# Kernel optimization log

Hardware: AMD Instinct MI355X
Metric: run time of the kernel (lower is better)

The kernel has to match this reference:

```python
import jax, jax.numpy as jnp
import numpy as np

B, S, D = 2, 2048, 1024
H = 16
HD = D // H  # 64

def setup_inputs() -> dict:
    key = jax.random.key(0)
    ks = jax.random.split(key, 5)
    scale = 0.02
    x = jax.random.normal(ks[0], (B, S, D), dtype=jnp.float32)
    w_attn = jax.random.normal(ks[1], (D, 3 * D), dtype=jnp.float32) * scale
    b_attn = jnp.zeros((3 * D,), dtype=jnp.float32)
    w_proj = jax.random.normal(ks[2], (D, D), dtype=jnp.float32) * scale
    b_proj = jnp.zeros((D,), dtype=jnp.float32)
    return {"x": x, "w_attn": w_attn, "b_attn": b_attn, "w_proj": w_proj, "b_proj": b_proj}

def reference(x, w_attn, b_attn, w_proj, b_proj):
    b, s, d = x.shape
    qkv = x @ w_attn + b_attn                      # [B,S,3D]
    q, k, v = jnp.split(qkv, 3, axis=-1)
    # [B,H,S,HD]
    q = q.reshape(b, s, H, HD).transpose(0, 2, 1, 3)
    k = k.reshape(b, s, H, HD).transpose(0, 2, 1, 3)
    v = v.reshape(b, s, H, HD).transpose(0, 2, 1, 3)
    scores = jnp.einsum('bhqd,bhkd->bhqk', q, k) * (1.0 / np.sqrt(HD))
    causal = jnp.tril(jnp.ones((s, s), dtype=bool))
    scores = jnp.where(causal[None, None], scores, -jnp.inf)
    attn = jax.nn.softmax(scores, axis=-1)
    out = jnp.einsum('bhqk,bhkd->bhqd', attn, v)   # [B,H,S,HD]
    out = out.transpose(0, 2, 1, 3).reshape(b, s, d)
    return out @ w_proj + b_proj
```

## Files before the change

kernel.cpp:

```cpp
#include <hip/hip_runtime.h>

#define B_  2
#define S_  2048
#define D_  1024
#define H_  16
#define HD_ 64
#define TD_ 3072
#define M_  (B_*S_)
#define NWORK_ 24

using bf16x8 = __attribute__((ext_vector_type(8))) short;
using bf16x4 = __attribute__((ext_vector_type(4))) short;
using f32x4  = __attribute__((ext_vector_type(4))) float;

typedef __attribute__((address_space(1))) unsigned int uint_g;
typedef __attribute__((address_space(3))) unsigned int uint_l;

#define MFMA32 __builtin_amdgcn_mfma_f32_16x16x32_bf16

#if defined(__has_builtin)
#if __has_builtin(__builtin_amdgcn_mfma_f32_16x16x16_bf16_1k)
#define MFMA16(a,b,c) __builtin_amdgcn_mfma_f32_16x16x16_bf16_1k(a,b,c,0,0,0)
#define HAVE_MFMA16 1
#elif __has_builtin(__builtin_amdgcn_mfma_f32_16x16x16bf16_1k)
#define MFMA16(a,b,c) __builtin_amdgcn_mfma_f32_16x16x16bf16_1k(a,b,c,0,0,0)
#define HAVE_MFMA16 1
#endif
#endif
#ifndef HAVE_MFMA16
static __device__ __forceinline__ f32x4 MFMA16_stub(bf16x4 a, bf16x4 b, f32x4 c) { return c; }
#define MFMA16(a,b,c) MFMA16_stub(a,b,c)
#endif

static __device__ __forceinline__ short f2bf(float f) {
    unsigned u = __float_as_uint(f);
    u += 0x7FFFu + ((u >> 16) & 1u);
    return (short)(u >> 16);
}
static __device__ __forceinline__ unsigned pack2bf(float a, float b) {
    return (unsigned)(unsigned short)f2bf(a) | ((unsigned)(unsigned short)f2bf(b) << 16);
}
static __device__ __forceinline__ void gload_lds16(const short* g, short* l) {
    __builtin_amdgcn_global_load_lds((const uint_g*)g, (uint_l*)l, 16, 0, 0);
}
static __device__ __forceinline__ void unpack8(uint4 u, float* f) {
    unsigned a0 = u.x, a1 = u.y, a2 = u.z, a3 = u.w;
    f[0] = __uint_as_float(a0 << 16); f[1] = __uint_as_float(a0 & 0xFFFF0000u);
    f[2] = __uint_as_float(a1 << 16); f[3] = __uint_as_float(a1 & 0xFFFF0000u);
    f[4] = __uint_as_float(a2 << 16); f[5] = __uint_as_float(a2 & 0xFFFF0000u);
    f[6] = __uint_as_float(a3 << 16); f[7] = __uint_as_float(a3 & 0xFFFF0000u);
}

__global__ __launch_bounds__(256)
void prep_kernel(const float* __restrict__ x, short* __restrict__ xb,
                 const float* __restrict__ w_attn, short* __restrict__ wat,
                 const float* __restrict__ w_proj, short* __restrict__ wpt) {
    __shared__ float T[32][33];
    const int bx = blockIdx.x;
    if (bx < 4096) {
        int i = bx * 256 + threadIdx.x;
        float4 v = *((const float4*)x + i);
        short4 o;
        o.x = f2bf(v.x); o.y = f2bf(v.y); o.z = f2bf(v.z); o.w = f2bf(v.w);
        *((short4*)xb + i) = o;
        return;
    }
    const float* W; short* Wt; int N, n0, k0;
    if (bx < 7168) { int b = bx - 4096; W = w_attn; Wt = wat; N = TD_; n0 = (b % 96) * 32; k0 = (b / 96) * 32; }
    else           { int b = bx - 7168; W = w_proj; Wt = wpt; N = D_;  n0 = (b % 32) * 32; k0 = (b / 32) * 32; }
    const int tx = threadIdx.x & 31, ty = threadIdx.x >> 5;
    #pragma unroll
    for (int i = 0; i < 4; ++i)
        T[ty + i * 8][tx] = W[(size_t)(k0 + ty + i * 8) * N + n0 + tx];
    __syncthreads();
    #pragma unroll
    for (int i = 0; i < 4; ++i)
        Wt[(size_t)(n0 + ty + i * 8) * D_ + k0 + tx] = f2bf(T[tx][ty + i * 8]);
}

__global__ __launch_bounds__(256)
void vtrans_kernel(const short* __restrict__ V, short* __restrict__ Vt) {
    __shared__ short T[32][33];
    int p  = blockIdx.z;
    int s0 = blockIdx.x * 32;
    int d0 = blockIdx.y * 32;
    int tx = threadIdx.x & 31, ty = threadIdx.x >> 5;
    const short* Vp  = V  + (size_t)p * S_ * HD_;
    short*       Vtp = Vt + (size_t)p * HD_ * S_;
    #pragma unroll
    for (int i = 0; i < 4; ++i)
        T[ty + i * 8][tx] = Vp[(s0 + ty + i * 8) * HD_ + d0 + tx];
    __syncthreads();
    #pragma unroll
    for (int i = 0; i < 4; ++i)
        Vtp[(size_t)(d0 + ty + i * 8) * S_ + s0 + tx] = T[tx][ty + i * 8];
}

__global__ __launch_bounds__(256, 3)
void gemm128_qkv_kernel(const short* __restrict__ A, const short* __restrict__ Bt,
                        const float* __restrict__ bias,
                        short* __restrict__ Qo, short* __restrict__ Ko, short* __restrict__ Vo,
                        int M, int N, int K) {
    __shared__ __align__(16) char lds[49152];

    const int tid  = threadIdx.x;
    const int w    = tid >> 6, lane = tid & 63;
    const int quad = lane >> 4, l16 = lane & 15;
    const int wm   = w >> 1,  wn  = w & 1;

    const int gx  = gridDim.x;
    const int nwg = gx * gridDim.y;
    const int bid = blockIdx.y * gx + blockIdx.x;
    const int sbid = (bid & 7) * (nwg >> 3) + (bid >> 3);
    const int rowBase = (sbid / gx) * 128;
    const int colBase = (sbid % gx) * 128;

    const int scol = ((lane & 3) * 8) ^ ((lane & 32) >> 1);
    const int sr0  = w * 32 + (lane >> 2);
    const short* Asrc0 = A  + (size_t)(rowBase + sr0)      * K + scol;
    const short* Asrc1 = A  + (size_t)(rowBase + sr0 + 16) * K + scol;
    const short* Bsrc0 = Bt + (size_t)(colBase + sr0)      * K + scol;
    const short* Bsrc1 = Bt + (size_t)(colBase + sr0 + 16) * K + scol;

    const int rterm = (l16 * 64 + quad * 16) ^ ((l16 & 8) << 2);
    const char* ArdBase = lds + wm * 4096 + rterm;
    const char* BrdBase = lds + 24576 + wn * 4096 + rterm;

#define STAGE_A(t) { int sl_ = ((t) % 3) * 8192; \
    gload_lds16(Asrc0 + (size_t)(t) * 32, (short*)(lds + sl_) + (w * 2)     * 512); \
    gload_lds16(Asrc1 + (size_t)(t) * 32, (short*)(lds + sl_) + (w * 2 + 1) * 512); }
#define STAGE_B(t) { int sl_ = 24576 + ((t) % 3) * 8192; \
    gload_lds16(Bsrc0 + (size_t)(t) * 32, (short*)(lds + sl_) + (w * 2)     * 512); \
    gload_lds16(Bsrc1 + (size_t)(t) * 32, (short*)(lds + sl_) + (w * 2 + 1) * 512); }

    f32x4 acc[4][4];
    const f32x4 zero = {0.f, 0.f, 0.f, 0.f};
    #pragma unroll
    for (int i = 0; i < 4; ++i)
        #pragma unroll
        for (int j = 0; j < 4; ++j) acc[i][j] = zero;

    const int nk = K >> 5;
    STAGE_A(0); STAGE_B(0);
    STAGE_A(1); STAGE_B(1);

    for (int t = 0; t < nk; ++t) {
        if (t + 1 < nk) { asm volatile("s_waitcnt vmcnt(4)" ::: "memory"); }
        else            { asm volatile("s_waitcnt vmcnt(0)" ::: "memory"); }
        __builtin_amdgcn_s_barrier();
        __builtin_amdgcn_sched_barrier(0);

        const int sl = (t % 3) * 8192;
        const char* Ab = ArdBase + sl;
        const char* Bb = BrdBase + sl;
        bf16x8 bfr[4], afr[4];
        #pragma unroll
        for (int ni = 0; ni < 4; ++ni) bfr[ni] = *(const bf16x8*)(Bb + ni * 1024);
        #pragma unroll
        for (int mi = 0; mi < 4; ++mi) afr[mi] = *(const bf16x8*)(Ab + mi * 1024);
        if (t + 2 < nk) { STAGE_A(t + 2); STAGE_B(t + 2); }

        __builtin_amdgcn_s_setprio(1);
        #pragma unroll
        for (int mi = 0; mi < 4; ++mi)
            #pragma unroll
            for (int ni = 0; ni < 4; ++ni)
                acc[mi][ni] = MFMA32(afr[mi], bfr[ni], acc[mi][ni], 0, 0, 0);
        __builtin_amdgcn_s_setprio(0);
    }
#undef STAGE_A
#undef STAGE_B

    #pragma unroll
    for (int ni = 0; ni < 4; ++ni) {
        int col = colBase + wn * 64 + ni * 16 + l16;
        int sel = col >> 10, cr = col & 1023;
        int h = cr >> 6, d = cr & 63;
        float bv  = bias[col];
        short* dst = (sel == 0) ? Qo : (sel == 1) ? Ko : Vo;
        float  scl = (sel == 0) ? 0.125f * 1.44269504f : 1.0f;
        #pragma unroll
        for (int mi = 0; mi < 4; ++mi) {
            int row = rowBase + wm * 64 + mi * 16 + quad * 4;
            #pragma unroll
            for (int r = 0; r < 4; ++r) {
                int rw = row + r;
                int bb = rw >> 11, s = rw & 2047;
                dst[((size_t)(bb * H_ + h) * S_ + s) * HD_ + d] =
                    f2bf((acc[mi][ni][r] + bv) * scl);
            }
        }
    }
}

__global__ __launch_bounds__(256, 2)
void gemm128_ring_kernel(const short* __restrict__ A, const short* __restrict__ Bt,
                         const float* __restrict__ bias, float* __restrict__ Cf,
                         int M, int N, int K) {
    __shared__ __align__(16) char lds[65536];

    const int tid  = threadIdx.x;
    const int w    = tid >> 6, lane = tid & 63;
    const int quad = lane >> 4, l16 = lane & 15;
    const int wm   = w >> 1,  wn  = w & 1;

    const int gx  = gridDim.x;
    const int nwg = gx * gridDim.y;
    const int bid = blockIdx.y * gx + blockIdx.x;
    const int sbid = (bid & 7) * (nwg >> 3) + (bid >> 3);
    const int rowBase = (sbid / gx) * 128;
    const int colBase = (sbid % gx) * 128;

    const int scol = ((lane & 3) * 8) ^ ((lane & 32) >> 1);
    const int sr0  = w * 32 + (lane >> 2);
    const short* Asrc0 = A  + (size_t)(rowBase + sr0)      * K + scol;
    const short* Asrc1 = A  + (size_t)(rowBase + sr0 + 16) * K + scol;
    const short* Bsrc0 = Bt + (size_t)(colBase + sr0)      * K + scol;
    const short* Bsrc1 = Bt + (size_t)(colBase + sr0 + 16) * K + scol;

    const int rterm = (l16 * 64 + quad * 16) ^ ((l16 & 8) << 2);
    const char* ArdBase = lds + wm * 4096 + rterm;
    const char* BrdBase = lds + 32768 + wn * 4096 + rterm;

#define STAGE_A(t) { int sl_ = ((t) & 3) * 8192; \
    gload_lds16(Asrc0 + (size_t)(t) * 32, (short*)(lds + sl_) + (w * 2)     * 512); \
    gload_lds16(Asrc1 + (size_t)(t) * 32, (short*)(lds + sl_) + (w * 2 + 1) * 512); }
#define STAGE_B(t) { int sl_ = 32768 + ((t) & 3) * 8192; \
    gload_lds16(Bsrc0 + (size_t)(t) * 32, (short*)(lds + sl_) + (w * 2)     * 512); \
    gload_lds16(Bsrc1 + (size_t)(t) * 32, (short*)(lds + sl_) + (w * 2 + 1) * 512); }

    f32x4 acc[4][4];
    const f32x4 zero = {0.f, 0.f, 0.f, 0.f};
    #pragma unroll
    for (int i = 0; i < 4; ++i)
        #pragma unroll
        for (int j = 0; j < 4; ++j) acc[i][j] = zero;

    const int nk = K >> 5;
    STAGE_A(0); STAGE_B(0);
    STAGE_A(1); STAGE_B(1);

    for (int t = 0; t < nk; ++t) {
        if (t + 1 < nk) { asm volatile("s_waitcnt vmcnt(4)" ::: "memory"); }
        else            { asm volatile("s_waitcnt vmcnt(0)" ::: "memory"); }
        __builtin_amdgcn_s_barrier();
        __builtin_amdgcn_sched_barrier(0);

        const char* Ab = ArdBase + (t & 3) * 8192;
        const char* Bb = BrdBase + (t & 3) * 8192;
        bf16x8 bfr[4], afr[4];
        #pragma unroll
        for (int ni = 0; ni < 4; ++ni) bfr[ni] = *(const bf16x8*)(Bb + ni * 1024);
        #pragma unroll
        for (int mi = 0; mi < 4; ++mi) afr[mi] = *(const bf16x8*)(Ab + mi * 1024);
        if (t + 2 < nk) { STAGE_A(t + 2); STAGE_B(t + 2); }

        __builtin_amdgcn_s_setprio(1);
        #pragma unroll
        for (int mi = 0; mi < 4; ++mi)
            #pragma unroll
            for (int ni = 0; ni < 4; ++ni)
                acc[mi][ni] = MFMA32(afr[mi], bfr[ni], acc[mi][ni], 0, 0, 0);
        __builtin_amdgcn_s_setprio(0);
    }
#undef STAGE_A
#undef STAGE_B

    #pragma unroll
    for (int mi = 0; mi < 4; ++mi) {
        int row = rowBase + wm * 64 + mi * 16 + quad * 4;
        #pragma unroll
        for (int ni = 0; ni < 4; ++ni) {
            int col = colBase + wn * 64 + ni * 16 + l16;
            float bv = bias[col];
            #pragma unroll
            for (int r = 0; r < 4; ++r)
                Cf[(size_t)(row + r) * N + col] = acc[mi][ni][r] + bv;
        }
    }
}

__global__ __launch_bounds__(256, 3)
void flash_mfma_kernel(const short* __restrict__ Qg, const short* __restrict__ Kg,
                       const short* __restrict__ Vtg,
                       short* __restrict__ pO, float* __restrict__ pl) {
    __shared__ __align__(16) short Ks[64][72];
    __shared__ __align__(16) short Vs[64][72];

    const int plane_id = blockIdx.x;
    const int y = blockIdx.y;
    int qi, kc;
    if (y < 8) { qi = y; kc = 0; }
    else       { qi = 8 + ((y - 8) >> 1); kc = (y - 8) & 1; }
    int nkt = 2 * qi + 2 - kc * 16;
    if (nkt > 16) nkt = 16;
    const int kvOrigin = kc * 1024;

    const int tid  = threadIdx.x;
    const int w    = tid >> 6, lane = tid & 63;
    const int quad = lane >> 4, l16 = lane & 15;
    const int qBase = qi * 128;
    const size_t plane = (size_t)plane_id * S_ * HD_;

    const int sr0 = tid >> 3;
    const int sc0 = (tid & 7) * 8;

    const int qsubA = qBase + w * 32;
    const short* QrowA = Qg + plane + (size_t)(qsubA + l16) * HD_ + quad * 8;
    const bf16x8 qa0 = *(const bf16x8*)(QrowA);
    const bf16x8 qa1 = *(const bf16x8*)(QrowA + 32);
    const short* QrowB = QrowA + 16 * HD_;
    const bf16x8 qb0 = *(const bf16x8*)(QrowB);
    const bf16x8 qb1 = *(const bf16x8*)(QrowB + 32);

    f32x4 oA[4], oB[4];
    const f32x4 zero = {0.f, 0.f, 0.f, 0.f};
    #pragma unroll
    for (int i = 0; i < 4; ++i) { oA[i] = zero; oB[i] = zero; }
    float lA = 0.f, lB = 0.f;
    const int q_globA = qsubA + l16;
    const int q_globB = qsubA + 16 + l16;
    const int q_wave_max = qsubA + 31;

    uint4 ka0, ka1, va0, va1;
    ka0 = *(const uint4*)(Kg  + plane + (size_t)(kvOrigin + sr0)      * HD_ + sc0);
    ka1 = *(const uint4*)(Kg  + plane + (size_t)(kvOrigin + sr0 + 32) * HD_ + sc0);
    va0 = *(const uint4*)(Vtg + plane + (size_t)sr0        * S_ + kvOrigin + sc0);
    va1 = *(const uint4*)(Vtg + plane + (size_t)(sr0 + 32) * S_ + kvOrigin + sc0);

    for (int j = 0; j < nkt; ++j) {
        __syncthreads();
        *(uint4*)&Ks[sr0][sc0]      = ka0;
        *(uint4*)&Ks[sr0 + 32][sc0] = ka1;
        *(uint4*)&Vs[sr0][sc0]      = va0;
        *(uint4*)&Vs[sr0 + 32][sc0] = va1;
        __syncthreads();

        if (j + 1 < nkt) {
            const int kvB = kvOrigin + (j + 1) * 64;
            ka0 = *(const uint4*)(Kg  + plane + (size_t)(kvB + sr0)      * HD_ + sc0);
            ka1 = *(const uint4*)(Kg  + plane + (size_t)(kvB + sr0 + 32) * HD_ + sc0);
            va0 = *(const uint4*)(Vtg + plane + (size_t)sr0        * S_ + kvB + sc0);
            va1 = *(const uint4*)(Vtg + plane + (size_t)(sr0 + 32) * S_ + kvB + sc0);
        }

        const int kvBase = kvOrigin + j * 64;
        if (kvBase > q_wave_max) continue;

        f32x4 sA[4], sB[4];
        __builtin_amdgcn_s_setprio(1);
        #pragma unroll
        for (int ct = 0; ct < 4; ++ct) {
            bf16x8 kf0 = *(const bf16x8*)&Ks[ct * 16 + l16][quad * 8];
            bf16x8 kf1 = *(const bf16x8*)&Ks[ct * 16 + l16][32 + quad * 8];
            f32x4 a = zero, b = zero;
            a = MFMA32(kf0, qa0, a, 0, 0, 0);
            a = MFMA32(kf1, qa1, a, 0, 0, 0);
            b = MFMA32(kf0, qb0, b, 0, 0, 0);
            b = MFMA32(kf1, qb1, b, 0, 0, 0);
            sA[ct] = a; sB[ct] = b;
        }
        __builtin_amdgcn_s_setprio(0);

        if (kvBase + 63 > qsubA) {
            #pragma unroll
            for (int ct = 0; ct < 4; ++ct) {
                int kv = kvBase + ct * 16 + quad * 4;
                #pragma unroll
                for (int r = 0; r < 4; ++r)
                    if (kv + r > q_globA) sA[ct][r] = -3.0e38f;
            }
        }
        if (kvBase + 63 > qsubA + 16) {
            #pragma unroll
            for (int ct = 0; ct < 4; ++ct) {
                int kv = kvBase + ct * 16 + quad * 4;
                #pragma unroll
                for (int r = 0; r < 4; ++r)
                    if (kv + r > q_globB) sB[ct][r] = -3.0e38f;
            }
        }

        #pragma unroll
        for (int ct = 0; ct < 4; ++ct) {
            float pa0 = __builtin_amdgcn_exp2f(sA[ct][0]), pa1 = __builtin_amdgcn_exp2f(sA[ct][1]);
            float pa2 = __builtin_amdgcn_exp2f(sA[ct][2]), pa3 = __builtin_amdgcn_exp2f(sA[ct][3]);
            float pb0 = __builtin_amdgcn_exp2f(sB[ct][0]), pb1 = __builtin_amdgcn_exp2f(sB[ct][1]);
            float pb2 = __builtin_amdgcn_exp2f(sB[ct][2]), pb3 = __builtin_amdgcn_exp2f(sB[ct][3]);
            lA += (pa0 + pa1) + (pa2 + pa3);
            lB += (pb0 + pb1) + (pb2 + pb3);
            bf16x4 pA, pB;
            *(unsigned*)&pA       = pack2bf(pa0, pa1);
            *((unsigned*)&pA + 1) = pack2bf(pa2, pa3);
            *(unsigned*)&pB       = pack2bf(pb0, pb1);
            *((unsigned*)&pB + 1) = pack2bf(pb2, pb3);
            __builtin_amdgcn_s_setprio(1);
            #pragma unroll
            for (int dt = 0; dt < 4; ++dt) {
                bf16x4 vfr = *(const bf16x4*)&Vs[dt * 16 + l16][ct * 16 + quad * 4];
                oA[dt] = MFMA16(vfr, pA, oA[dt]);
                oB[dt] = MFMA16(vfr, pB, oB[dt]);
            }
            __builtin_amdgcn_s_setprio(0);
        }
    }

    lA += __shfl_xor(lA, 16); lA += __shfl_xor(lA, 32);
    lB += __shfl_xor(lB, 16); lB += __shfl_xor(lB, 32);
    const size_t lbase = ((size_t)plane_id * NWORK_ + y) * 128 + w * 32;
    if (quad == 0) {
        pl[lbase + l16]      = lA;
        pl[lbase + 16 + l16] = lB;
    }

    __syncthreads();
    short* Pw = (w < 2) ? &Ks[w * 32][0] : &Vs[(w - 2) * 32][0];
    #pragma unroll
    for (int dt = 0; dt < 4; ++dt) {
        uint2 ua, ub;
        ua.x = pack2bf(oA[dt][0], oA[dt][1]);
        ua.y = pack2bf(oA[dt][2], oA[dt][3]);
        ub.x = pack2bf(oB[dt][0], oB[dt][1]);
        ub.y = pack2bf(oB[dt][2], oB[dt][3]);
        *(uint2*)&Pw[l16 * 72 + dt * 16 + quad * 4]        = ua;
        *(uint2*)&Pw[(16 + l16) * 72 + dt * 16 + quad * 4] = ub;
    }
    __builtin_amdgcn_s_waitcnt(0xC07F);
    short* outBase = pO + (((size_t)plane_id * NWORK_ + y) * 128 + w * 32) * 64;
    #pragma unroll
    for (int pass = 0; pass < 4; ++pass) {
        int r  = pass * 8 + (lane >> 3);
        int cs = (lane & 7) * 8;
        uint4 vv = *(const uint4*)&Pw[r * 72 + cs];
        *(uint4*)(outBase + r * 64 + cs) = vv;
    }
}

__global__ __launch_bounds__(256)
void reduce_kernel(const short* __restrict__ pO, const float* __restrict__ pl,
                   short* __restrict__ atb) {
    const int plane_id = blockIdx.x, qi = blockIdx.y;
    const int h = plane_id & (H_ - 1), b = plane_id >> 4;
    const int tid = threadIdx.x;
    const int row = tid >> 1;
    const int cb  = (tid & 1) * 32;

    int t0, nch;
    if (qi < 8) { t0 = qi; nch = 1; }
    else        { t0 = 8 + 2 * (qi - 8); nch = 2; }

    const size_t pbase = (((size_t)plane_id * NWORK_ + t0) * 128 + row) * 64 + cb;
    float f[32], g[8];
    unpack8(*(const uint4*)(pO + pbase),      f);
    unpack8(*(const uint4*)(pO + pbase + 8),  f + 8);
    unpack8(*(const uint4*)(pO + pbase + 16), f + 16);
    unpack8(*(const uint4*)(pO + pbase + 24), f + 24);
    float l = pl[((size_t)plane_id * NWORK_ + t0) * 128 + row];
    if (nch == 2) {
        #pragma unroll
        for (int c = 0; c < 4; ++c) {
            unpack8(*(const uint4*)(pO + pbase + 8192 + c * 8), g);
            #pragma unroll
            for (int i = 0; i < 8; ++i) f[c * 8 + i] += g[i];
        }
        l += pl[((size_t)plane_id * NWORK_ + t0 + 1) * 128 + row];
    }
    const float inv = 1.0f / l;
    short* dst = atb + (size_t)(b * S_ + qi * 128 + row) * D_ + h * HD_ + cb;
    #pragma unroll
    for (int c = 0; c < 4; ++c) {
        uint2 o2;
        o2.x = pack2bf(f[c * 8 + 0] * inv, f[c * 8 + 1] * inv);
        o2.y = pack2bf(f[c * 8 + 2] * inv, f[c * 8 + 3] * inv);
        uint2 o3;
        o3.x = pack2bf(f[c * 8 + 4] * inv, f[c * 8 + 5] * inv);
        o3.y = pack2bf(f[c * 8 + 6] * inv, f[c * 8 + 7] * inv);
        uint4 ov; ov.x = o2.x; ov.y = o2.y; ov.z = o3.x; ov.w = o3.y;
        *(uint4*)(dst + c * 8) = ov;
    }
}

extern "C" void kernel_launch(void* const* d_in, const int* in_sizes, int n_in,
                              void* d_out, int out_size, void* d_ws, size_t ws_size,
                              hipStream_t stream) {
    const float* x      = (const float*)d_in[0];
    const float* w_attn = (const float*)d_in[1];
    const float* b_attn = (const float*)d_in[2];
    const float* w_proj = (const float*)d_in[3];
    const float* b_proj = (const float*)d_in[4];
    float* out = (float*)d_out;

    char* ws = (char*)d_ws;
    short* xb  = (short*)ws; ws += (size_t)M_ * D_ * 2;
    short* wat = (short*)ws; ws += (size_t)TD_ * D_ * 2;
    short* wpt = (short*)ws; ws += (size_t)D_ * D_ * 2;
    short* qg  = (short*)ws; ws += (size_t)M_ * D_ * 2;
    short* kg  = (short*)ws; ws += (size_t)M_ * D_ * 2;
    short* vg  = (short*)ws; ws += (size_t)M_ * D_ * 2;
    short* vtg = (short*)ws; ws += (size_t)M_ * D_ * 2;
    short* atb = (short*)ws; ws += (size_t)M_ * D_ * 2;

    short* pO = (short*)d_ws;
    float* pl = (float*)((char*)d_ws + (size_t)32 * NWORK_ * 128 * 64 * 2);

    prep_kernel<<<8192, 256, 0, stream>>>(x, xb, w_attn, wat, w_proj, wpt);

    gemm128_qkv_kernel<<<dim3(TD_ / 128, M_ / 128), 256, 0, stream>>>(
        xb, wat, b_attn, qg, kg, vg, M_, TD_, D_);

    vtrans_kernel<<<dim3(S_ / 32, HD_ / 32, B_ * H_), 256, 0, stream>>>(vg, vtg);

    flash_mfma_kernel<<<dim3(B_ * H_, NWORK_), 256, 0, stream>>>(qg, kg, vtg, pO, pl);

    reduce_kernel<<<dim3(B_ * H_, S_ / 128), 256, 0, stream>>>(pO, pl, atb);

    gemm128_ring_kernel<<<dim3(D_ / 128, M_ / 128), 256, 0, stream>>>(
        atb, wpt, b_proj, out, M_, D_, D_);
}
```

Measured before the change: 176.0 us.

## Narrow output-projection GEMM tiles and double-buffer K/V in flash kernel

The output projection GEMM now uses 128x64 tiles with a three-slot LDS ring and occupancy 4, doubling the grid from 256 to 512 workgroups so more CUs stay busy. The flash attention kernel double-buffers its K/V LDS tiles, writing tile j+1 while tile j is computed, which drops one barrier per iteration. This trades extra LDS per block and more A-tile reloads in the GEMM for better overlap and occupancy.

```diff
diff --git a/kernel.cpp b/kernel.cpp
--- a/kernel.cpp
+++ b/kernel.cpp
@@ -193,11 +193,11 @@
     }
 }
 
-__global__ __launch_bounds__(256, 2)
-void gemm128_ring_kernel(const short* __restrict__ A, const short* __restrict__ Bt,
-                         const float* __restrict__ bias, float* __restrict__ Cf,
-                         int M, int N, int K) {
-    __shared__ __align__(16) char lds[65536];
+__global__ __launch_bounds__(256, 4)
+void gemm_op_kernel(const short* __restrict__ A, const short* __restrict__ Bt,
+                    const float* __restrict__ bias, float* __restrict__ Cf,
+                    int M, int N, int K) {
+    __shared__ __align__(16) char lds[36864];
 
     const int tid  = threadIdx.x;
     const int w    = tid >> 6, lane = tid & 63;
@@ -209,48 +209,47 @@
     const int bid = blockIdx.y * gx + blockIdx.x;
     const int sbid = (bid & 7) * (nwg >> 3) + (bid >> 3);
     const int rowBase = (sbid / gx) * 128;
-    const int colBase = (sbid % gx) * 128;
+    const int colBase = (sbid % gx) * 64;
 
     const int scol = ((lane & 3) * 8) ^ ((lane & 32) >> 1);
-    const int sr0  = w * 32 + (lane >> 2);
-    const short* Asrc0 = A  + (size_t)(rowBase + sr0)      * K + scol;
-    const short* Asrc1 = A  + (size_t)(rowBase + sr0 + 16) * K + scol;
-    const short* Bsrc0 = Bt + (size_t)(colBase + sr0)      * K + scol;
-    const short* Bsrc1 = Bt + (size_t)(colBase + sr0 + 16) * K + scol;
+    const int srA  = w * 32 + (lane >> 2);
+    const int srB  = w * 16 + (lane >> 2);
+    const short* Asrc0 = A  + (size_t)(rowBase + srA)      * K + scol;
+    const short* Asrc1 = A  + (size_t)(rowBase + srA + 16) * K + scol;
+    const short* Bsrc0 = Bt + (size_t)(colBase + srB)      * K + scol;
 
     const int rterm = (l16 * 64 + quad * 16) ^ ((l16 & 8) << 2);
     const char* ArdBase = lds + wm * 4096 + rterm;
-    const char* BrdBase = lds + 32768 + wn * 4096 + rterm;
-
-#define STAGE_A(t) { int sl_ = ((t) & 3) * 8192; \
+    const char* BrdBase = lds + 24576 + wn * 2048 + rterm;
+
+#define STAGE_A(t) { int sl_ = ((t) % 3) * 8192; \
     gload_lds16(Asrc0 + (size_t)(t) * 32, (short*)(lds + sl_) + (w * 2)     * 512); \
     gload_lds16(Asrc1 + (size_t)(t) * 32, (short*)(lds + sl_) + (w * 2 + 1) * 512); }
-#define STAGE_B(t) { int sl_ = 32768 + ((t) & 3) * 8192; \
-    gload_lds16(Bsrc0 + (size_t)(t) * 32, (short*)(lds + sl_) + (w * 2)     * 512); \
-    gload_lds16(Bsrc1 + (size_t)(t) * 32, (short*)(lds + sl_) + (w * 2 + 1) * 512); }
-
-    f32x4 acc[4][4];
+#define STAGE_B(t) { int sl_ = 24576 + ((t) % 3) * 4096; \
+    gload_lds16(Bsrc0 + (size_t)(t) * 32, (short*)(lds + sl_) + w * 512); }
+
+    f32x4 acc[4][2];
     const f32x4 zero = {0.f, 0.f, 0.f, 0.f};
     #pragma unroll
     for (int i = 0; i < 4; ++i)
         #pragma unroll
-        for (int j = 0; j < 4; ++j) acc[i][j] = zero;
+        for (int j = 0; j < 2; ++j) acc[i][j] = zero;
 
     const int nk = K >> 5;
     STAGE_A(0); STAGE_B(0);
     STAGE_A(1); STAGE_B(1);
 
     for (int t = 0; t < nk; ++t) {
-        if (t + 1 < nk) { asm volatile("s_waitcnt vmcnt(4)" ::: "memory"); }
+        if (t + 1 < nk) { asm volatile("s_waitcnt vmcnt(3)" ::: "memory"); }
         else            { asm volatile("s_waitcnt vmcnt(0)" ::: "memory"); }
         __builtin_amdgcn_s_barrier();
         __builtin_amdgcn_sched_barrier(0);
 
-        const char* Ab = ArdBase + (t & 3) * 8192;
-        const char* Bb = BrdBase + (t & 3) * 8192;
-        bf16x8 bfr[4], afr[4];
-        #pragma unroll
-        for (int ni = 0; ni < 4; ++ni) bfr[ni] = *(const bf16x8*)(Bb + ni * 1024);
+        const char* Ab = ArdBase + (t % 3) * 8192;
+        const char* Bb = BrdBase + (t % 3) * 4096;
+        bf16x8 bfr[2], afr[4];
+        #pragma unroll
+        for (int ni = 0; ni < 2; ++ni) bfr[ni] = *(const bf16x8*)(Bb + ni * 1024);
         #pragma unroll
         for (int mi = 0; mi < 4; ++mi) afr[mi] = *(const bf16x8*)(Ab + mi * 1024);
         if (t + 2 < nk) { STAGE_A(t + 2); STAGE_B(t + 2); }
@@ -259,7 +258,7 @@
         #pragma unroll
         for (int mi = 0; mi < 4; ++mi)
             #pragma unroll
-            for (int ni = 0; ni < 4; ++ni)
+            for (int ni = 0; ni < 2; ++ni)
                 acc[mi][ni] = MFMA32(afr[mi], bfr[ni], acc[mi][ni], 0, 0, 0);
         __builtin_amdgcn_s_setprio(0);
     }
@@ -270,8 +269,8 @@
     for (int mi = 0; mi < 4; ++mi) {
         int row = rowBase + wm * 64 + mi * 16 + quad * 4;
         #pragma unroll
-        for (int ni = 0; ni < 4; ++ni) {
-            int col = colBase + wn * 64 + ni * 16 + l16;
+        for (int ni = 0; ni < 2; ++ni) {
+            int col = colBase + wn * 32 + ni * 16 + l16;
             float bv = bias[col];
             #pragma unroll
             for (int r = 0; r < 4; ++r)
@@ -284,8 +283,8 @@
 void flash_mfma_kernel(const short* __restrict__ Qg, const short* __restrict__ Kg,
                        const short* __restrict__ Vtg,
                        short* __restrict__ pO, float* __restrict__ pl) {
-    __shared__ __align__(16) short Ks[64][72];
-    __shared__ __align__(16) short Vs[64][72];
+    __shared__ __align__(16) short Ks[2][64][72];
+    __shared__ __align__(16) short Vs[2][64][72];
 
     const int plane_id = blockIdx.x;
     const int y = blockIdx.y;
@@ -327,82 +326,96 @@
     ka1 = *(const uint4*)(Kg  + plane + (size_t)(kvOrigin + sr0 + 32) * HD_ + sc0);
     va0 = *(const uint4*)(Vtg + plane + (size_t)sr0        * S_ + kvOrigin + sc0);
     va1 = *(const uint4*)(Vtg + plane + (size_t)(sr0 + 32) * S_ + kvOrigin + sc0);
+    *(uint4*)&Ks[0][sr0][sc0]      = ka0;
+    *(uint4*)&Ks[0][sr0 + 32][sc0] = ka1;
+    *(uint4*)&Vs[0][sr0][sc0]      = va0;
+    *(uint4*)&Vs[0][sr0 + 32][sc0] = va1;
+    if (nkt > 1) {
+        const int kvB = kvOrigin + 64;
+        ka0 = *(const uint4*)(Kg  + plane + (size_t)(kvB + sr0)      * HD_ + sc0);
+        ka1 = *(const uint4*)(Kg  + plane + (size_t)(kvB + sr0 + 32) * HD_ + sc0);
+        va0 = *(const uint4*)(Vtg + plane + (size_t)sr0        * S_ + kvB + sc0);
+        va1 = *(const uint4*)(Vtg + plane + (size_t)(sr0 + 32) * S_ + kvB + sc0);
+    }
+    __syncthreads();
 
     for (int j = 0; j < nkt; ++j) {
-        __syncthreads();
-        *(uint4*)&Ks[sr0][sc0]      = ka0;
-        *(uint4*)&Ks[sr0 + 32][sc0] = ka1;
-        *(uint4*)&Vs[sr0][sc0]      = va0;
-        *(uint4*)&Vs[sr0 + 32][sc0] = va1;
-        __syncthreads();
-
         if (j + 1 < nkt) {
-            const int kvB = kvOrigin + (j + 1) * 64;
-            ka0 = *(const uint4*)(Kg  + plane + (size_t)(kvB + sr0)      * HD_ + sc0);
-            ka1 = *(const uint4*)(Kg  + plane + (size_t)(kvB + sr0 + 32) * HD_ + sc0);
-            va0 = *(const uint4*)(Vtg + plane + (size_t)sr0        * S_ + kvB + sc0);
-            va1 = *(const uint4*)(Vtg + plane + (size_t)(sr0 + 32) * S_ + kvB + sc0);
-        }
-
-        const int kvBase = kvOrigin + j * 64;
-        if (kvBase > q_wave_max) continue;
-
-        f32x4 sA[4], sB[4];
-        __builtin_amdgcn_s_setprio(1);
-        #pragma unroll
-        for (int ct = 0; ct < 4; ++ct) {
-            bf16x8 kf0 = *(const bf16x8*)&Ks[ct * 16 + l16][quad * 8];
-            bf16x8 kf1 = *(const bf16x8*)&Ks[ct * 16 + l16][32 + quad * 8];
-            f32x4 a = zero, b = zero;
-            a = MFMA32(kf0, qa0, a, 0, 0, 0);
-            a = MFMA32(kf1, qa1, a, 0, 0, 0);
-            b = MFMA32(kf0, qb0, b, 0, 0, 0);
-            b = MFMA32(kf1, qb1, b, 0, 0, 0);
-            sA[ct] = a; sB[ct] = b;
-        }
-        __builtin_amdgcn_s_setprio(0);
-
-        if (kvBase + 63 > qsubA) {
-            #pragma unroll
-            for (int ct = 0; ct < 4; ++ct) {
-                int kv = kvBase + ct * 16 + quad * 4;
-                #pragma unroll
-                for (int r = 0; r < 4; ++r)
-                    if (kv + r > q_globA) sA[ct][r] = -3.0e38f;
+            const int bb = (j + 1) & 1;
+            *(uint4*)&Ks[bb][sr0][sc0]      = ka0;
+            *(uint4*)&Ks[bb][sr0 + 32][sc0] = ka1;
+            *(uint4*)&Vs[bb][sr0][sc0]      = va0;
+            *(uint4*)&Vs[bb][sr0 + 32][sc0] = va1;
+            if (j + 2 < nkt) {
+                const int kvB = kvOrigin + (j + 2) * 64;
+                ka0 = *(const uint4*)(Kg  + plane + (size_t)(kvB + sr0)      * HD_ + sc0);
+                ka1 = *(const uint4*)(Kg  + plane + (size_t)(kvB + sr0 + 32) * HD_ + sc0);
+                va0 = *(const uint4*)(Vtg + plane + (size_t)sr0        * S_ + kvB + sc0);
+                va1 = *(const uint4*)(Vtg + plane + (size_t)(sr0 + 32) * S_ + kvB + sc0);
             }
         }
-        if (kvBase + 63 > qsubA + 16) {
+
+        const int cb = j & 1;
+        const int kvBase = kvOrigin + j * 64;
+        if (kvBase <= q_wave_max) {
+            f32x4 sA[4], sB[4];
+            __builtin_amdgcn_s_setprio(1);
             #pragma unroll
             for (int ct = 0; ct < 4; ++ct) {
-                int kv = kvBase + ct * 16 + quad * 4;
+                bf16x8 kf0 = *(const bf16x8*)&Ks[cb][ct * 16 + l16][quad * 8];
+                bf16x8 kf1 = *(const bf16x8*)&Ks[cb][ct * 16 + l16][32 + quad * 8];
+                f32x4 a = zero, b = zero;
+                a = MFMA32(kf0, qa0, a, 0, 0, 0);
+                a = MFMA32(kf1, qa1, a, 0, 0, 0);
+                b = MFMA32(kf0, qb0, b, 0, 0, 0);
+                b = MFMA32(kf1, qb1, b, 0, 0, 0);
+                sA[ct] = a; sB[ct] = b;
+            }
+            __builtin_amdgcn_s_setprio(0);
+
+            if (kvBase + 63 > qsubA) {
                 #pragma unroll
-                for (int r = 0; r < 4; ++r)
-                    if (kv + r > q_globB) sB[ct][r] = -3.0e38f;
+                for (int ct = 0; ct < 4; ++ct) {
+                    int kv = kvBase + ct * 16 + quad * 4;
+                    #pragma unroll
+                    for (int r = 0; r < 4; ++r)
+                        if (kv + r > q_globA) sA[ct][r] = -3.0e38f;
+                }
+            }
+            if (kvBase + 63 > qsubA + 16) {
+                #pragma unroll
+                for (int ct = 0; ct < 4; ++ct) {
+                    int kv = kvBase + ct * 16 + quad * 4;
+                    #pragma unroll
+                    for (int r = 0; r < 4; ++r)
+                        if (kv + r > q_globB) sB[ct][r] = -3.0e38f;
+                }
+            }
+
+            #pragma unroll
+            for (int ct = 0; ct < 4; ++ct) {
+                float pa0 = __builtin_amdgcn_exp2f(sA[ct][0]), pa1 = __builtin_amdgcn_exp2f(sA[ct][1]);
+                float pa2 = __builtin_amdgcn_exp2f(sA[ct][2]), pa3 = __builtin_amdgcn_exp2f(sA[ct][3]);
+                float pb0 = __builtin_amdgcn_exp2f(sB[ct][0]), pb1 = __builtin_amdgcn_exp2f(sB[ct][1]);
+                float pb2 = __builtin_amdgcn_exp2f(sB[ct][2]), pb3 = __builtin_amdgcn_exp2f(sB[ct][3]);
+                lA += (pa0 + pa1) + (pa2 + pa3);
+                lB += (pb0 + pb1) + (pb2 + pb3);
+                bf16x4 pA, pB;
+                *(unsigned*)&pA       = pack2bf(pa0, pa1);
+                *((unsigned*)&pA + 1) = pack2bf(pa2, pa3);
+                *(unsigned*)&pB       = pack2bf(pb0, pb1);
+                *((unsigned*)&pB + 1) = pack2bf(pb2, pb3);
+                __builtin_amdgcn_s_setprio(1);
+                #pragma unroll
+                for (int dt = 0; dt < 4; ++dt) {
+                    bf16x4 vfr = *(const bf16x4*)&Vs[cb][dt * 16 + l16][ct * 16 + quad * 4];
+                    oA[dt] = MFMA16(vfr, pA, oA[dt]);
+                    oB[dt] = MFMA16(vfr, pB, oB[dt]);
+                }
+                __builtin_amdgcn_s_setprio(0);
             }
         }
-
-        #pragma unroll
-        for (int ct = 0; ct < 4; ++ct) {
-            float pa0 = __builtin_amdgcn_exp2f(sA[ct][0]), pa1 = __builtin_amdgcn_exp2f(sA[ct][1]);
-            float pa2 = __builtin_amdgcn_exp2f(sA[ct][2]), pa3 = __builtin_amdgcn_exp2f(sA[ct][3]);
-            float pb0 = __builtin_amdgcn_exp2f(sB[ct][0]), pb1 = __builtin_amdgcn_exp2f(sB[ct][1]);
-            float pb2 = __builtin_amdgcn_exp2f(sB[ct][2]), pb3 = __builtin_amdgcn_exp2f(sB[ct][3]);
-            lA += (pa0 + pa1) + (pa2 + pa3);
-            lB += (pb0 + pb1) + (pb2 + pb3);
-            bf16x4 pA, pB;
-            *(unsigned*)&pA       = pack2bf(pa0, pa1);
-            *((unsigned*)&pA + 1) = pack2bf(pa2, pa3);
-            *(unsigned*)&pB       = pack2bf(pb0, pb1);
-            *((unsigned*)&pB + 1) = pack2bf(pb2, pb3);
-            __builtin_amdgcn_s_setprio(1);
-            #pragma unroll
-            for (int dt = 0; dt < 4; ++dt) {
-                bf16x4 vfr = *(const bf16x4*)&Vs[dt * 16 + l16][ct * 16 + quad * 4];
-                oA[dt] = MFMA16(vfr, pA, oA[dt]);
-                oB[dt] = MFMA16(vfr, pB, oB[dt]);
-            }
-            __builtin_amdgcn_s_setprio(0);
-        }
+        __syncthreads();
     }
 
     lA += __shfl_xor(lA, 16); lA += __shfl_xor(lA, 32);
@@ -413,8 +426,7 @@
         pl[lbase + 16 + l16] = lB;
     }
 
-    __syncthreads();
-    short* Pw = (w < 2) ? &Ks[w * 32][0] : &Vs[(w - 2) * 32][0];
+    short* Pw = (w < 2) ? &Ks[0][w * 32][0] : &Vs[0][(w - 2) * 32][0];
     #pragma unroll
     for (int dt = 0; dt < 4; ++dt) {
         uint2 ua, ub;
@@ -514,6 +526,6 @@
 
     reduce_kernel<<<dim3(B_ * H_, S_ / 128), 256, 0, stream>>>(pO, pl, atb);
 
-    gemm128_ring_kernel<<<dim3(D_ / 128, M_ / 128), 256, 0, stream>>>(
+    gemm_op_kernel<<<dim3(D_ / 64, M_ / 128), 256, 0, stream>>>(
         atb, wpt, b_proj, out, M_, D_, D_);
 }
```

Result: slower. 179.8 us (+2.2%).
